# Optimization experiments

Hardware: AMD Instinct MI355X
Metric: run time of the kernel (lower is better)

Reference implementation:

```python
import jax, jax.numpy as jnp
import numpy as np
from jax.scipy.linalg import expm

B, S, D, E, K, NROT = 2, 2048, 1024, 8, 2, 3
EPS = 1e-5


def setup_inputs() -> dict:
    key = jax.random.key(0)
    ks = jax.random.split(key, 16)
    sc = 0.02
    x = jax.random.normal(ks[0], (B, S, D), jnp.float32)
    ln_gamma = 1.0 + sc * jax.random.normal(ks[1], (D,), jnp.float32)
    ln_beta = sc * jax.random.normal(ks[2], (D,), jnp.float32)
    abel_w = sc * jax.random.normal(ks[3], (D, D), jnp.float32)
    abel_b = sc * jax.random.normal(ks[4], (D,), jnp.float32)
    moe_gate_w = sc * jax.random.normal(ks[5], (D, E), jnp.float32)
    moe_gate_b = sc * jax.random.normal(ks[6], (E,), jnp.float32)
    ew1 = sc * jax.random.normal(ks[7], (E, D, 2 * D), jnp.float32)
    eb1 = sc * jax.random.normal(ks[8], (E, 2 * D), jnp.float32)
    ew2 = sc * jax.random.normal(ks[9], (E, 2 * D, D), jnp.float32)
    eb2 = sc * jax.random.normal(ks[10], (E, D), jnp.float32)
    g = sc * jax.random.normal(ks[11], (NROT, D, D), jnp.float32)
    gens = 0.5 * (g - jnp.swapaxes(g, -1, -2))  # skew-symmetric, as in reset_parameters
    gc_w = sc * jax.random.normal(ks[12], (2 * D, 1), jnp.float32)
    gc_b = sc * jax.random.normal(ks[13], (1,), jnp.float32)
    return dict(x=x, ln_gamma=ln_gamma, ln_beta=ln_beta, abel_w=abel_w, abel_b=abel_b,
                moe_gate_w=moe_gate_w, moe_gate_b=moe_gate_b, ew1=ew1, eb1=eb1,
                ew2=ew2, eb2=eb2, gens=gens, gc_w=gc_w, gc_b=gc_b)


def _gelu(x):
    return jax.nn.gelu(x, approximate=False)  # torch nn.GELU default = exact erf


def _forward(x, ln_gamma, ln_beta, abel_w, abel_b, moe_gate_w, moe_gate_b,
             ew1, eb1, ew2, eb2, gens, gc_w, gc_b):
    residual = x
    # LayerNorm
    mu = jnp.mean(x, axis=-1, keepdims=True)
    var = jnp.mean((x - mu) ** 2, axis=-1, keepdims=True)
    xn = (x - mu) * jax.lax.rsqrt(var + EPS) * ln_gamma + ln_beta
    # abel branch: Linear + GELU
    abel_out = _gelu(xn @ abel_w + abel_b)
    # MoE: dense all-experts compute, masked by top-k softmax weights
    logits = xn @ moe_gate_w + moe_gate_b                      # [B,S,E]
    topw, topi = jax.lax.top_k(logits, K)                      # [B,S,K]
    topw = jax.nn.softmax(topw, axis=-1)
    w_dense = jnp.sum(jax.nn.one_hot(topi, E, dtype=xn.dtype) * topw[..., None], axis=-2)  # [B,S,E]
    h = _gelu(jnp.einsum('bsd,edh->ebsh', xn, ew1) + eb1[:, None, None, :])  # [E,B,S,2D]
    eo = jnp.einsum('ebsh,ehd->ebsd', h, ew2) + eb2[:, None, None, :]        # [E,B,S,D]
    moe_out = jnp.einsum('ebsd,bse->bsd', eo, w_dense)
    # GeometricRotation: sequential matrix_exp rotations
    for i in range(NROT):
        moe_out = moe_out @ expm(gens[i])
    # gated residual mix
    combined = jnp.concatenate([abel_out, moe_out], axis=-1)
    gate = jax.nn.sigmoid(combined @ gc_w + gc_b)              # [B,S,1]
    mixed = abel_out * (1.0 - gate) + moe_out * gate
    return residual + mixed


def reference(x, ln_gamma, ln_beta, abel_w, abel_b, moe_gate_w, moe_gate_b,
              ew1, eb1, ew2, eb2, gens, gc_w, gc_b):
    return _forward(x, ln_gamma, ln_beta, abel_w, abel_b, moe_gate_w, moe_gate_b,
                    ew1, eb1, ew2, eb2, gens, gc_w, gc_b)
```

## Files before the change

kernel.cpp:

```cpp
#include <hip/hip_runtime.h>
#include <hip/hip_bf16.h>
#include <cstdint>
#include <cstddef>

#define DD   1024
#define DD2  2048
#define EE   8
#define NTOK 4096
#define CAPR 10240
#define MAXT1 72
#define MAXT2 56

typedef __bf16 bf16_t;
typedef __bf16 bf16x8 __attribute__((ext_vector_type(8)));
typedef __bf16 bf16x4 __attribute__((ext_vector_type(4)));
typedef float  f32x4v __attribute__((ext_vector_type(4)));

__device__ __forceinline__ float gelu_f(float v){
  const float t = v*(0.7978845608028654f + 0.0356774081f*v*v);
  const float u = __expf(2.0f*t);
  return __fdividef(v*u, 1.0f + u);
}

__device__ __forceinline__ void gload_lds16(const void* g, void* l){
  __builtin_amdgcn_global_load_lds(
    (const __attribute__((address_space(1))) unsigned int*)(uintptr_t)g,
    (__attribute__((address_space(3))) unsigned int*)(uintptr_t)l,
    16, 0, 0);
}

enum { EPI_GELU_F32=0, EPI_GELU_BF16=1, EPI_BIAS_BF16=2, EPI_SCALE_BF16=3,
       EPI_ADDV_BF16=4, EPI_BF16=5, EPI_F32=6 };

template<int BM,int BN,int WAVES,int EPI,bool TAB>
__global__ __launch_bounds__(WAVES*64)
void gemm_bt(const bf16_t* __restrict__ A, const bf16_t* __restrict__ Bt,
             const int N, const int K, const int gx, const int gy, const int gz,
             const long sAz, const long sBz, const long sOz,
             const int* __restrict__ tileE, const int* __restrict__ tileR,
             const int* __restrict__ ntp, const int* __restrict__ offp,
             const int* __restrict__ tokOf,
             const float* __restrict__ bias, const long sBias,
             const float alpha,
             const bf16_t* __restrict__ addv,
             const bf16_t* __restrict__ abelB, const float* __restrict__ abelBias,
             bf16_t* __restrict__ abelOut, const int aN, const int aGx,
             float* __restrict__ outF, bf16_t* __restrict__ outB)
{
  constexpr int BK = 32;
  constexpr int WROWS = WAVES/2;
  constexpr int WM = BM/WROWS, WN = BN/2;
  constexpr int FM = WM/16, FN = WN/16;
  constexpr int IA = BM/(16*WAVES), IB = BN/(16*WAVES);
  constexpr int NLD = IA + IB;
  __shared__ alignas(16) bf16_t sA[3][BM*BK];
  __shared__ alignas(16) bf16_t sB[3][BN*BK];

  int bx, by, bz; long ro = 0;
  if constexpr (TAB) {
    const int nwg = gx * gy;
    const int q = nwg >> 3, r = nwg & 7;
    const int k = blockIdx.x & 7, i = blockIdx.x >> 3;
    if (i >= q + (k < r ? 1 : 0)) return;
    const int l = k * q + (k < r ? k : r) + i;
    const int ti = l / gx; bx = l - ti*gx;
    if (ti >= ntp[0]) return;
    bz = tileE[ti]; by = 0;
    if (bz == EE) { if (bx >= aGx) return; ro = tileR[ti]; }
    else          { ro = (long)offp[bz] + tileR[ti]; }
  } else {
    const int nwg = gx * gy * gz;
    const int q = nwg >> 3, r = nwg & 7;
    const int k = blockIdx.x & 7, i = blockIdx.x >> 3;
    if (i >= q + (k < r ? 1 : 0)) return;
    const int l = k * q + (k < r ? k : r) + i;
    bx = l % gx; const int t2 = l / gx; by = t2 % gy; bz = t2 / gy;
  }

  const int z = bz;
  const bool abelT = TAB && (z == EE);
  int NN = abelT ? aN : N;
  const bool useTok = TAB && !abelT && (tokOf != nullptr);
  const bf16_t* Bp;
  const float*  bp;
  float*  oF = outF;
  bf16_t* oB;
  if (abelT) {
    Bp = abelB; bp = abelBias;
    oB = abelOut + ro * (long)aN;
  } else if constexpr (TAB) {
    Bp = Bt + (size_t)z * sBz;
    bp = bias ? bias + (size_t)z * sBias : nullptr;
    oB = outB + ro * (long)N;
  } else {
    Bp = Bt + (size_t)z * sBz;
    bp = bias ? bias + (size_t)z * sBias : nullptr;
    A += (size_t)z * sAz;
    oB = outB; if (oB) oB += (size_t)z * sOz;
    if (oF) oF += (size_t)z * sOz;
  }
  const bf16_t* vp = addv ? addv + (size_t)z * sOz : nullptr;

  const int tid = threadIdx.x;
  const int wid = tid >> 6, lid = tid & 63;
  const int wr = wid >> 1, wc = wid & 1;
  const int brow = (TAB ? 0 : by * BM), bcol = bx * BN;
  const int fr = lid & 15, fq = lid >> 4;
  const int rl = lid >> 2, qs = lid & 3;

  const char* aSrc[IA];
  const char* bSrc[IB];
  #pragma unroll
  for (int i = 0; i < IA; i++) {
    const int rloc = (wid*IA + i)*16 + rl;
    const int q = qs ^ ((rloc >> 1) & 3);
    const bf16_t* arow;
    if constexpr (TAB) {
      arow = useTok ? (A + (size_t)tokOf[ro + rloc] * K)
                    : (A + (size_t)(ro + rloc) * K);
    } else {
      arow = A + (size_t)(brow + rloc) * K;
    }
    aSrc[i] = (const char*)arow + q*16;
  }
  #pragma unroll
  for (int i = 0; i < IB; i++) {
    const int rloc = (wid*IB + i)*16 + rl;
    const int q = qs ^ ((rloc >> 1) & 3);
    bSrc[i] = (const char*)(Bp + (size_t)(bcol + rloc) * K) + q*16;
  }

  f32x4v acc[FM][FN] = {};

  auto stage = [&](int buf, int kt) {
    #pragma unroll
    for (int i = 0; i < IA; i++)
      gload_lds16(aSrc[i] + (size_t)kt*2, (char*)sA[buf] + (wid*IA + i)*1024);
    #pragma unroll
    for (int i = 0; i < IB; i++)
      gload_lds16(bSrc[i] + (size_t)kt*2, (char*)sB[buf] + (wid*IB + i)*1024);
  };

  stage(0, 0);
  stage(1, BK);
  const int nk = K / BK;
  int b0 = 0, b1 = 1, b2 = 2;

  for (int t = 0; t < nk; ++t) {
    if (t < nk - 1) asm volatile("s_waitcnt vmcnt(%0)" :: "i"(NLD) : "memory");
    else            asm volatile("s_waitcnt vmcnt(0)" ::: "memory");
    __builtin_amdgcn_s_barrier();
    __builtin_amdgcn_sched_barrier(0);
    if (t + 2 < nk) stage(b2, (t + 2)*BK);

    bf16x8 af[FM], bb[FN];
    #pragma unroll
    for (int mi = 0; mi < FM; mi++) {
      const int r2 = wr*WM + mi*16 + fr;
      const int q = fq ^ ((r2 >> 1) & 3);
      af[mi] = *(const bf16x8*)((const char*)sA[b0] + r2*64 + q*16);
    }
    #pragma unroll
    for (int ni = 0; ni < FN; ni++) {
      const int r2 = wc*WN + ni*16 + fr;
      const int q = fq ^ ((r2 >> 1) & 3);
      bb[ni] = *(const bf16x8*)((const char*)sB[b0] + r2*64 + q*16);
    }
    #pragma unroll
    for (int mi = 0; mi < FM; mi++)
      #pragma unroll
      for (int ni = 0; ni < FN; ni++)
        acc[mi][ni] = __builtin_amdgcn_mfma_f32_16x16x32_bf16(
            af[mi], bb[ni], acc[mi][ni], 0, 0, 0);

    const int tb_ = b0; b0 = b1; b1 = b2; b2 = tb_;
  }

  #pragma unroll
  for (int mi = 0; mi < FM; mi++) {
    #pragma unroll
    for (int ni = 0; ni < FN; ni++) {
      const int rg0 = brow + wr*WM + mi*16 + fq*4;
      const int cg  = bcol + wc*WN + ni*16 + fr;
      #pragma unroll
      for (int i = 0; i < 4; i++) {
        const int rg = rg0 + i;
        float v = acc[mi][ni][i];
        if constexpr (EPI == EPI_GELU_F32) {
          v += bp[cg];
          oF[(size_t)rg*NN + cg] = gelu_f(v);
        } else if constexpr (EPI == EPI_GELU_BF16) {
          v += bp[cg];
          oB[(size_t)rg*NN + cg] = (bf16_t)gelu_f(v);
        } else if constexpr (EPI == EPI_BIAS_BF16) {
          v += bp[cg];
          oB[(size_t)rg*NN + cg] = (bf16_t)v;
        } else if constexpr (EPI == EPI_SCALE_BF16) {
          oB[(size_t)rg*NN + cg] = (bf16_t)(v * alpha);
        } else if constexpr (EPI == EPI_ADDV_BF16) {
          oB[(size_t)rg*NN + cg] = (bf16_t)(v + (float)vp[(size_t)rg*NN + cg]);
        } else if constexpr (EPI == EPI_BF16) {
          oB[(size_t)rg*NN + cg] = (bf16_t)v;
        } else {
          oF[(size_t)rg*NN + cg] = v;
        }
      }
    }
  }
}

struct TRef { const float* src; bf16_t* dst; int R, C, bx, by; };

__device__ __forceinline__ TRef resolve256(
    int ti, const float* abel_w, bf16_t* abel_wT,
    const float* ew1, bf16_t* ew1T, const float* ew2, bf16_t* ew2T){
  TRef tr;
  if (ti < 64) {
    tr.src = abel_w; tr.dst = abel_wT; tr.R = DD; tr.C = DD;
    tr.bx = ti & 15; tr.by = ti >> 4;
  } else if (ti < 1088) {
    const int i = ti - 64, z = i >> 7, r = i & 127;
    tr.src = ew1 + (size_t)z*DD*DD2; tr.dst = ew1T + (size_t)z*DD2*DD;
    tr.R = DD; tr.C = DD2; tr.bx = r & 31; tr.by = r >> 5;
  } else {
    const int i = ti - 1088, z = i >> 7, r = i & 127;
    tr.src = ew2 + (size_t)z*DD2*DD; tr.dst = ew2T + (size_t)z*DD*DD2;
    tr.R = DD2; tr.C = DD; tr.bx = r & 15; tr.by = r >> 4;
  }
  return tr;
}

__global__ __launch_bounds__(256)
void pre_kernel(const float* __restrict__ x, const float* __restrict__ gamma,
                const float* __restrict__ beta, const float* __restrict__ gw,
                const float* __restrict__ gb,
                bf16_t* __restrict__ xnb, int2* __restrict__ ids,
                float2* __restrict__ wts,
                const float* __restrict__ abel_w, bf16_t* __restrict__ abel_wT,
                const float* __restrict__ ew1, bf16_t* __restrict__ ew1T,
                const float* __restrict__ ew2, bf16_t* __restrict__ ew2T,
                const float* __restrict__ gens, bf16_t* __restrict__ Hn)
{
  __shared__ bf16_t tb[64][260];
  __shared__ float redS[4], redQ[4], mv[2], pr[32];
  const int bid = blockIdx.x, tid = threadIdx.x;

  if (bid < 4096) {
    const int t = bid, j0 = tid*4;
    const int wid = tid >> 6, lid = tid & 63;
    const float4 v = *(const float4*)(x + (size_t)t*DD + j0);
    float s  = v.x + v.y + v.z + v.w;
    float ss = v.x*v.x + v.y*v.y + v.z*v.z + v.w*v.w;
    #pragma unroll
    for (int off = 32; off; off >>= 1) { s += __shfl_down(s, off); ss += __shfl_down(ss, off); }
    if (lid == 0) { redS[wid] = s; redQ[wid] = ss; }
    __syncthreads();
    if (tid == 0) {
      const float S1 = redS[0]+redS[1]+redS[2]+redS[3];
      const float S2 = redQ[0]+redQ[1]+redQ[2]+redQ[3];
      const float mu  = S1 * (1.0f/DD);
      const float var = S2 * (1.0f/DD) - mu*mu;
      mv[0] = mu; mv[1] = rsqrtf(var + 1e-5f);
    }
    __syncthreads();
    const float mu = mv[0], rstd = mv[1];
    const float4 g = *(const float4*)(gamma + j0);
    const float4 b = *(const float4*)(beta  + j0);
    float xn[4];
    xn[0] = (v.x-mu)*rstd*g.x + b.x;
    xn[1] = (v.y-mu)*rstd*g.y + b.y;
    xn[2] = (v.z-mu)*rstd*g.z + b.z;
    xn[3] = (v.w-mu)*rstd*g.w + b.w;
    bf16x4 ov; ov[0]=(bf16_t)xn[0]; ov[1]=(bf16_t)xn[1]; ov[2]=(bf16_t)xn[2]; ov[3]=(bf16_t)xn[3];
    *(bf16x4*)(xnb + (size_t)t*DD + j0) = ov;

    float p[8] = {0,0,0,0,0,0,0,0};
    #pragma unroll
    for (int i = 0; i < 4; i++) {
      const float4 a0 = *(const float4*)(gw + (size_t)(j0+i)*EE);
      const float4 a1 = *(const float4*)(gw + (size_t)(j0+i)*EE + 4);
      const float xv = xn[i];
      p[0]+=xv*a0.x; p[1]+=xv*a0.y; p[2]+=xv*a0.z; p[3]+=xv*a0.w;
      p[4]+=xv*a1.x; p[5]+=xv*a1.y; p[6]+=xv*a1.z; p[7]+=xv*a1.w;
    }
    #pragma unroll
    for (int off = 32; off; off >>= 1) {
      #pragma unroll
      for (int e = 0; e < 8; e++) p[e] += __shfl_down(p[e], off);
    }
    if (lid == 0) {
      #pragma unroll
      for (int e = 0; e < 8; e++) pr[wid*8 + e] = p[e];
    }
    __syncthreads();
    if (tid == 0) {
      float l[8];
      #pragma unroll
      for (int e = 0; e < 8; e++) l[e] = pr[e] + pr[8+e] + pr[16+e] + pr[24+e] + gb[e];
      int i1 = 0; float m1 = l[0];
      #pragma unroll
      for (int e = 1; e < 8; e++) if (l[e] > m1) { m1 = l[e]; i1 = e; }
      int i2 = 0; float m2 = -1e30f;
      #pragma unroll
      for (int e = 0; e < 8; e++) if (e != i1 && l[e] > m2) { m2 = l[e]; i2 = e; }
      const float wa = 1.0f/(1.0f + expf(m2 - m1));
      ids[t] = make_int2(i1, i2);
      wts[t] = make_float2(wa, 1.0f - wa);
    }
  } else if (bid < 6208) {
    const TRef tr = resolve256(bid - 4096, abel_w, abel_wT, ew1, ew1T, ew2, ew2T);
    const int lx = tid & 15, ly = tid >> 4;
    const int r0 = tr.by*256, c0 = tr.bx*64;
    #pragma unroll
    for (int i = 0; i < 16; i++) {
      const int r = ly + i*16;
      const float4 v = *(const float4*)(tr.src + (size_t)(r0 + r)*tr.C + c0 + lx*4);
      tb[lx*4+0][r] = (bf16_t)v.x;
      tb[lx*4+1][r] = (bf16_t)v.y;
      tb[lx*4+2][r] = (bf16_t)v.z;
      tb[lx*4+3][r] = (bf16_t)v.w;
    }
    __syncthreads();
    const int w = tid >> 6, l = tid & 63;
    #pragma unroll
    for (int i = 0; i < 16; i++) {
      const int c = w*16 + i;
      const bf16x4 o = *(const bf16x4*)(&tb[c][l*4]);
      *(bf16x4*)(tr.dst + (size_t)(c0 + c)*tr.R + r0 + l*4) = o;
    }
  } else {
    #pragma unroll
    for (int it = 0; it < 4; it++) {
      const long i4 = (((long)(bid - 6208)*4 + it)*256 + tid)*4;
      const float4 v = *(const float4*)(gens + i4);
      bf16x4 b; b[0]=(bf16_t)(-v.x); b[1]=(bf16_t)(-v.y);
      b[2]=(bf16_t)(-v.z); b[3]=(bf16_t)(-v.w);
      *(bf16x4*)(Hn + i4) = b;
    }
  }
}

__global__ __launch_bounds__(256)
void tb16_kernel(const bf16_t* __restrict__ Ut, bf16_t* __restrict__ Tb){
  __shared__ bf16_t tile[32][33];
  const bf16_t* src = Ut + (size_t)(1 - blockIdx.z) * DD * DD;
  bf16_t*       dst = Tb + (size_t)blockIdx.z * DD * DD;
  const int c0 = blockIdx.x*32, r0 = blockIdx.y*32;
  #pragma unroll
  for (int i = 0; i < 4; i++)
    tile[threadIdx.y + i*8][threadIdx.x] = src[(size_t)(r0 + threadIdx.y + i*8)*DD + c0 + threadIdx.x];
  __syncthreads();
  #pragma unroll
  for (int i = 0; i < 4; i++)
    dst[(size_t)(c0 + threadIdx.y + i*8)*DD + r0 + threadIdx.x] = tile[threadIdx.x][threadIdx.y + i*8];
}

__global__ __launch_bounds__(256)
void vw_kernel(const bf16_t* __restrict__ Hn, const bf16_t* __restrict__ H2,
               bf16_t* __restrict__ Vb, bf16_t* __restrict__ Wtb){
  const long i0 = ((long)blockIdx.x*256 + threadIdx.x)*4;
  const long rc = i0 % (long)(DD*DD);
  const int r = (int)(rc / DD), c0 = (int)(rc % DD);
  const bf16x4 h  = *(const bf16x4*)(Hn + i0);
  const bf16x4 h2 = *(const bf16x4*)(H2 + i0);
  bf16x4 v, w;
  #pragma unroll
  for (int j = 0; j < 4; j++) {
    const float d  = (r == c0 + j) ? 1.0f : 0.0f;
    const float fh = (float)h[j], f2 = (float)h2[j];
    v[j] = (bf16_t)(d + fh + f2*0.5f);
    w[j] = (bf16_t)(d*(1.0f/6.0f) - fh*(1.0f/24.0f) + f2*(1.0f/120.0f));
  }
  *(bf16x4*)(Vb  + i0) = v;
  *(bf16x4*)(Wtb + i0) = w;
}

__global__ __launch_bounds__(256)
void route_kernel(const int2* __restrict__ ids, int* __restrict__ slotA,
                  int* __restrict__ slotB, int* __restrict__ cnt,
                  int* __restrict__ off, int* __restrict__ tE1,
                  int* __restrict__ tR1, int* __restrict__ tE2,
                  int* __restrict__ tR2, int* __restrict__ ntp)
{
  const int tid = threadIdx.x;
  const int wid = tid >> 6, lid = tid & 63;
  __shared__ int wsum[EE][4];
  __shared__ int base[EE];
  if (tid < EE) base[tid] = 0;
  __syncthreads();
  const unsigned long long lt = (1ull << lid) - 1ull;
  for (int c0 = 0; c0 < NTOK; c0 += 256) {
    const int t = c0 + tid;
    const int2 id = ids[t];
    int pA = 0, pB = 0;
    #pragma unroll
    for (int e = 0; e < EE; e++) {
      const bool fA = (id.x == e), fB = (id.y == e);
      const unsigned long long mA = __ballot(fA);
      const unsigned long long mB = __ballot(fB);
      const int cA = __popcll(mA);
      if (lid == 0) wsum[e][wid] = cA + __popcll(mB);
      if (fA) pA = __popcll(mA & lt);
      if (fB) pB = cA + __popcll(mB & lt);
    }
    __syncthreads();
    int wbA = base[id.x], wbB = base[id.y];
    for (int w = 0; w < wid; w++) { wbA += wsum[id.x][w]; wbB += wsum[id.y][w]; }
    slotA[t] = wbA + pA;
    slotB[t] = wbB + pB;
    __syncthreads();
    if (tid < EE) base[tid] += wsum[tid][0]+wsum[tid][1]+wsum[tid][2]+wsum[tid][3];
    __syncthreads();
  }
  if (tid == 0) {
    int a = 0, n1 = 0, n2 = 0;
    for (int e = 0; e < EE; e++) {
      cnt[e] = base[e]; off[e] = a;
      for (int r2 = 0; r2 < base[e]; r2 += 128) { tE1[n1] = e; tR1[n1] = r2; n1++; }
      for (int r2 = 0; r2 < base[e]; r2 += 256) { tE2[n2] = e; tR2[n2] = r2; n2++; }
      a += (base[e] + 255) & ~255;
    }
    for (int m = 0; m < NTOK/256; m++) { tE2[n2] = EE; tR2[n2] = m*256; n2++; }
    ntp[0] = n1; ntp[1] = n2;
  }
}

__global__ __launch_bounds__(256)
void fill_tok_kernel(const int2* __restrict__ ids, const int* __restrict__ slotA,
                     const int* __restrict__ slotB, const int* __restrict__ off,
                     const int* __restrict__ cnt, int* __restrict__ tokOf){
  const int t = blockIdx.x*256 + threadIdx.x;
  const int2 id = ids[t];
  tokOf[off[id.x] + slotA[t]] = t;
  tokOf[off[id.y] + slotB[t]] = t;
  if (blockIdx.x == 0) {
    for (int e = 0; e < EE; e++) {
      const int c = cnt[e], o = off[e], al = (c + 255) & ~255;
      for (int p = c + threadIdx.x; p < al; p += 256) tokOf[o + p] = 0;
    }
  }
}

__global__ __launch_bounds__(256)
void combine_kernel(const bf16_t* __restrict__ Yg, const int2* __restrict__ ids,
                    const int* __restrict__ slotA, const int* __restrict__ slotB,
                    const int* __restrict__ off, const float2* __restrict__ wts,
                    bf16_t* __restrict__ Xa){
  const int t = blockIdx.x, j = threadIdx.x*4;
  const int2 id = ids[t];
  const float2 w = wts[t];
  const bf16x4 a = *(const bf16x4*)(Yg + (size_t)(off[id.x] + slotA[t])*DD + j);
  const bf16x4 b = *(const bf16x4*)(Yg + (size_t)(off[id.y] + slotB[t])*DD + j);
  bf16x4 o;
  #pragma unroll
  for (int i = 0; i < 4; i++) o[i] = (bf16_t)(w.x*(float)a[i] + w.y*(float)b[i]);
  *(bf16x4*)(Xa + (size_t)t*DD + j) = o;
}

__global__ __launch_bounds__(256)
void mix_kernel(const float* __restrict__ x, const bf16_t* __restrict__ abel,
                const float* __restrict__ rot, const float* __restrict__ gcw,
                const float* __restrict__ gcb, float* __restrict__ out)
{
  const int t = blockIdx.x, tid = threadIdx.x, j0 = tid*4;
  const int wid = tid >> 6, lid = tid & 63;
  const bf16x4 ab = *(const bf16x4*)(abel + (size_t)t*DD + j0);
  const float4 r  = *(const float4*)(rot  + (size_t)t*DD + j0);
  const float4 ga = *(const float4*)(gcw + j0);
  const float4 gr = *(const float4*)(gcw + DD + j0);
  const float a0 = (float)ab[0], a1 = (float)ab[1], a2 = (float)ab[2], a3 = (float)ab[3];
  float p = a0*ga.x + a1*ga.y + a2*ga.z + a3*ga.w
          + r.x*gr.x + r.y*gr.y + r.z*gr.z + r.w*gr.w;
  #pragma unroll
  for (int off = 32; off; off >>= 1) p += __shfl_down(p, off);
  __shared__ float red[4];
  __shared__ float gsh;
  if (lid == 0) red[wid] = p;
  __syncthreads();
  if (tid == 0) {
    const float P = red[0] + red[1] + red[2] + red[3] + gcb[0];
    gsh = 1.0f/(1.0f + expf(-P));
  }
  __syncthreads();
  const float gate = gsh, g1 = 1.0f - gate;
  const float4 xv = *(const float4*)(x + (size_t)t*DD + j0);
  float4 o;
  o.x = xv.x + a0*g1 + r.x*gate;
  o.y = xv.y + a1*g1 + r.y*gate;
  o.z = xv.z + a2*g1 + r.z*gate;
  o.w = xv.w + a3*g1 + r.w*gate;
  *(float4*)(out + (size_t)t*DD + j0) = o;
}

extern "C" void kernel_launch(void* const* d_in, const int* in_sizes, int n_in,
                              void* d_out, int out_size, void* d_ws, size_t ws_size,
                              hipStream_t stream)
{
  (void)in_sizes; (void)n_in; (void)out_size; (void)ws_size;
  const float* x      = (const float*)d_in[0];
  const float* ln_g   = (const float*)d_in[1];
  const float* ln_b   = (const float*)d_in[2];
  const float* abel_w = (const float*)d_in[3];
  const float* abel_b = (const float*)d_in[4];
  const float* gate_w = (const float*)d_in[5];
  const float* gate_b = (const float*)d_in[6];
  const float* ew1    = (const float*)d_in[7];
  const float* eb1    = (const float*)d_in[8];
  const float* ew2    = (const float*)d_in[9];
  const float* eb2    = (const float*)d_in[10];
  const float* gens   = (const float*)d_in[11];
  const float* gc_w   = (const float*)d_in[12];
  const float* gc_b   = (const float*)d_in[13];
  float* out = (float*)d_out;

  char* wsp = (char*)d_ws;
  auto alloc = [&](size_t bytes) -> char* {
    char* p = wsp; wsp += (bytes + 255) & ~(size_t)255; return p;
  };
  const size_t MB = 1u<<20;
  bf16_t* xnb   = (bf16_t*)alloc((size_t)NTOK*DD*2);
  int2*   ids   = (int2*)  alloc((size_t)NTOK*8);
  float2* wts   = (float2*)alloc((size_t)NTOK*8);
  int*    slotA = (int*)   alloc((size_t)NTOK*4);
  int*    slotB = (int*)   alloc((size_t)NTOK*4);
  int*    cnt   = (int*)   alloc(64);
  int*    off   = (int*)   alloc(64);
  int*    tE1   = (int*)   alloc(MAXT1*4);
  int*    tR1   = (int*)   alloc(MAXT1*4);
  int*    tE2   = (int*)   alloc(MAXT2*4);
  int*    tR2   = (int*)   alloc(MAXT2*4);
  int*    ntp   = (int*)   alloc(64);
  int*    tokOf = (int*)   alloc((size_t)CAPR*4);
  bf16_t* abel_wT = (bf16_t*)alloc((size_t)DD*DD*2);
  char*   UN      = alloc(64*MB);
  bf16_t* ew1T  = (bf16_t*)UN;
  bf16_t* ew2T  = (bf16_t*)(UN + 32*MB);
  bf16_t* Hn    = (bf16_t*)alloc((size_t)3*DD*DD*2);
  bf16_t* abelo = (bf16_t*)alloc((size_t)NTOK*DD*2);
  bf16_t* Yg    = (bf16_t*)alloc((size_t)CAPR*DD*2);
  bf16_t* Hg    = (bf16_t*)alloc((size_t)CAPR*DD2*2);
  bf16_t* Xa    = (bf16_t*)alloc((size_t)NTOK*DD*2);
  float*  rot   = (float*)Hg;
  bf16_t* H2  = (bf16_t*)(UN + 0*MB);
  bf16_t* H3  = (bf16_t*)(UN + 6*MB);
  bf16_t* Vb  = (bf16_t*)(UN + 12*MB);
  bf16_t* Wtb = (bf16_t*)(UN + 18*MB);
  bf16_t* Ut  = (bf16_t*)(UN + 24*MB);
  bf16_t* Tb  = (bf16_t*)(UN + 30*MB);
  bf16_t* Pb  = (bf16_t*)(UN + 34*MB);
  bf16_t* Rt  = (bf16_t*)(UN + 36*MB);
  const long D2 = (long)DD*DD;

  auto gflat = [](int gx, int gy, int gz) {
    const int nwg = gx*gy*gz; return 8 * ((nwg + 7) / 8);
  };

  pre_kernel<<<dim3(6976,1,1), 256, 0, stream>>>(
      x, ln_g, ln_b, gate_w, gate_b, xnb, ids, wts,
      abel_w, abel_wT, ew1, ew1T, ew2, ew2T, gens, Hn);

  route_kernel<<<dim3(1,1,1), 256, 0, stream>>>(ids, slotA, slotB, cnt, off,
                                                tE1, tR1, tE2, tR2, ntp);
  fill_tok_kernel<<<dim3(NTOK/256,1,1), 256, 0, stream>>>(ids, slotA, slotB, off, cnt, tokOf);

  gemm_bt<256,128,8,EPI_GELU_BF16,true><<<dim3(gflat(DD2/128, MAXT2, 1),1,1), 512, 0, stream>>>(
      xnb, ew1T, DD2, DD, DD2/128, MAXT2, 1, 0, (long)DD2*DD, 0,
      tE2, tR2, ntp + 1, off, tokOf, eb1, DD2, 1.0f, nullptr,
      abel_wT, abel_b, abelo, DD, DD/128, nullptr, Hg);
  gemm_bt<128,128,4,EPI_BIAS_BF16,true><<<dim3(gflat(DD/128, MAXT1, 1),1,1), 256, 0, stream>>>(
      Hg, ew2T, DD, DD2, DD/128, MAXT1, 1, 0, (long)DD*DD2, 0,
      tE1, tR1, ntp, off, nullptr, eb2, DD, 1.0f, nullptr,
      nullptr, nullptr, nullptr, 0, 0, nullptr, Yg);
  combine_kernel<<<dim3(NTOK,1,1), 256, 0, stream>>>(Yg, ids, slotA, slotB, off, wts, Xa);

  gemm_bt<64,64,4,EPI_SCALE_BF16,false><<<dim3(gflat(16,16,3),1,1), 256, 0, stream>>>(
      Hn, Hn, DD, DD, 16, 16, 3, D2, D2, D2, nullptr, nullptr, nullptr, nullptr,
      nullptr, nullptr, 0, -1.0f, nullptr,
      nullptr, nullptr, nullptr, 0, 0, nullptr, H2);
  gemm_bt<64,64,4,EPI_SCALE_BF16,false><<<dim3(gflat(16,16,3),1,1), 256, 0, stream>>>(
      H2, Hn, DD, DD, 16, 16, 3, D2, D2, D2, nullptr, nullptr, nullptr, nullptr,
      nullptr, nullptr, 0, -1.0f, nullptr,
      nullptr, nullptr, nullptr, 0, 0, nullptr, H3);
  vw_kernel<<<dim3(3*DD*DD/1024,1,1), 256, 0, stream>>>(Hn, H2, Vb, Wtb);
  gemm_bt<64,64,4,EPI_ADDV_BF16,false><<<dim3(gflat(16,16,3),1,1), 256, 0, stream>>>(
      H3, Wtb, DD, DD, 16, 16, 3, D2, D2, D2, nullptr, nullptr, nullptr, nullptr,
      nullptr, nullptr, 0, 1.0f, Vb,
      nullptr, nullptr, nullptr, 0, 0, nullptr, Ut);
  tb16_kernel<<<dim3(32,32,2), dim3(32,8,1), 0, stream>>>(Ut, Tb);
  gemm_bt<64,64,4,EPI_BF16,false><<<dim3(gflat(16,16,1),1,1), 256, 0, stream>>>(
      Ut + 2*D2, Tb, DD, DD, 16, 16, 1, 0, 0, 0, nullptr, nullptr, nullptr, nullptr,
      nullptr, nullptr, 0, 1.0f, nullptr,
      nullptr, nullptr, nullptr, 0, 0, nullptr, Pb);
  gemm_bt<64,64,4,EPI_BF16,false><<<dim3(gflat(16,16,1),1,1), 256, 0, stream>>>(
      Pb, Tb + D2, DD, DD, 16, 16, 1, 0, 0, 0, nullptr, nullptr, nullptr, nullptr,
      nullptr, nullptr, 0, 1.0f, nullptr,
      nullptr, nullptr, nullptr, 0, 0, nullptr, Rt);
  gemm_bt<128,128,4,EPI_F32,false><<<dim3(gflat(8,32,1),1,1), 256, 0, stream>>>(
      Xa, Rt, DD, DD, 8, 32, 1, 0, 0, 0, nullptr, nullptr, nullptr, nullptr,
      nullptr, nullptr, 0, 1.0f, nullptr,
      nullptr, nullptr, nullptr, 0, 0, rot, nullptr);

  mix_kernel<<<dim3(NTOK,1,1), 256, 0, stream>>>(x, abelo, rot, gc_w, gc_b, out);
}
```

Before: 341.1 us.

## Split prologue into weight-transpose and LayerNorm/gate kernels; retile rotation GEMM

```diff
diff --git a/kernel.cpp b/kernel.cpp
--- a/kernel.cpp
+++ b/kernel.cpp
@@ -209,134 +209,52 @@
   }
 }
 
-struct TRef { const float* src; bf16_t* dst; int R, C, bx, by; };
-
-__device__ __forceinline__ TRef resolve256(
-    int ti, const float* abel_w, bf16_t* abel_wT,
-    const float* ew1, bf16_t* ew1T, const float* ew2, bf16_t* ew2T){
-  TRef tr;
-  if (ti < 64) {
-    tr.src = abel_w; tr.dst = abel_wT; tr.R = DD; tr.C = DD;
-    tr.bx = ti & 15; tr.by = ti >> 4;
-  } else if (ti < 1088) {
-    const int i = ti - 64, z = i >> 7, r = i & 127;
-    tr.src = ew1 + (size_t)z*DD*DD2; tr.dst = ew1T + (size_t)z*DD2*DD;
-    tr.R = DD; tr.C = DD2; tr.bx = r & 31; tr.by = r >> 5;
+__device__ __forceinline__ void tcvt_tile(const float* __restrict__ src,
+                                          bf16_t* __restrict__ dst,
+                                          int R, int C, int bx, int by,
+                                          float (*t)[65]){
+  const int c0 = bx*64, r0 = by*64;
+  const int lx = threadIdx.x & 15, ly = threadIdx.x >> 4;
+  #pragma unroll
+  for (int i = 0; i < 4; i++) {
+    const int row = r0 + ly + i*16;
+    const float4 v = *(const float4*)(src + (size_t)row*C + c0 + lx*4);
+    t[ly + i*16][lx*4+0] = v.x; t[ly + i*16][lx*4+1] = v.y;
+    t[ly + i*16][lx*4+2] = v.z; t[ly + i*16][lx*4+3] = v.w;
+  }
+  __syncthreads();
+  #pragma unroll
+  for (int i = 0; i < 4; i++) {
+    const int c = c0 + ly + i*16;
+    bf16x4 o;
+    #pragma unroll
+    for (int j = 0; j < 4; j++) o[j] = (bf16_t)t[lx*4+j][ly + i*16];
+    *(bf16x4*)(dst + (size_t)c*R + r0 + lx*4) = o;
+  }
+}
+
+__global__ __launch_bounds__(256)
+void prep_kernel(const float* __restrict__ abel_w, bf16_t* __restrict__ abel_wT,
+                 const float* __restrict__ ew1, bf16_t* __restrict__ ew1T,
+                 const float* __restrict__ ew2, bf16_t* __restrict__ ew2T,
+                 const float* __restrict__ gens, bf16_t* __restrict__ Hn)
+{
+  __shared__ float t[64][65];
+  const int bid = blockIdx.x;
+  if (bid < 256) {
+    tcvt_tile(abel_w, abel_wT, DD, DD, bid & 15, bid >> 4, t);
+  } else if (bid < 4352) {
+    const int i = bid - 256, z = i >> 9, r = i & 511;
+    tcvt_tile(ew1 + (size_t)z*DD*DD2, ew1T + (size_t)z*DD2*DD, DD, DD2, r & 31, r >> 5, t);
+  } else if (bid < 8448) {
+    const int i = bid - 4352, z = i >> 9, r = i & 511;
+    tcvt_tile(ew2 + (size_t)z*DD2*DD, ew2T + (size_t)z*DD*DD2, DD2, DD, r & 15, r >> 4, t);
   } else {
-    const int i = ti - 1088, z = i >> 7, r = i & 127;
-    tr.src = ew2 + (size_t)z*DD2*DD; tr.dst = ew2T + (size_t)z*DD*DD2;
-    tr.R = DD2; tr.C = DD; tr.bx = r & 15; tr.by = r >> 4;
-  }
-  return tr;
-}
-
-__global__ __launch_bounds__(256)
-void pre_kernel(const float* __restrict__ x, const float* __restrict__ gamma,
-                const float* __restrict__ beta, const float* __restrict__ gw,
-                const float* __restrict__ gb,
-                bf16_t* __restrict__ xnb, int2* __restrict__ ids,
-                float2* __restrict__ wts,
-                const float* __restrict__ abel_w, bf16_t* __restrict__ abel_wT,
-                const float* __restrict__ ew1, bf16_t* __restrict__ ew1T,
-                const float* __restrict__ ew2, bf16_t* __restrict__ ew2T,
-                const float* __restrict__ gens, bf16_t* __restrict__ Hn)
-{
-  __shared__ bf16_t tb[64][260];
-  __shared__ float redS[4], redQ[4], mv[2], pr[32];
-  const int bid = blockIdx.x, tid = threadIdx.x;
-
-  if (bid < 4096) {
-    const int t = bid, j0 = tid*4;
-    const int wid = tid >> 6, lid = tid & 63;
-    const float4 v = *(const float4*)(x + (size_t)t*DD + j0);
-    float s  = v.x + v.y + v.z + v.w;
-    float ss = v.x*v.x + v.y*v.y + v.z*v.z + v.w*v.w;
-    #pragma unroll
-    for (int off = 32; off; off >>= 1) { s += __shfl_down(s, off); ss += __shfl_down(ss, off); }
-    if (lid == 0) { redS[wid] = s; redQ[wid] = ss; }
-    __syncthreads();
-    if (tid == 0) {
-      const float S1 = redS[0]+redS[1]+redS[2]+redS[3];
-      const float S2 = redQ[0]+redQ[1]+redQ[2]+redQ[3];
-      const float mu  = S1 * (1.0f/DD);
-      const float var = S2 * (1.0f/DD) - mu*mu;
-      mv[0] = mu; mv[1] = rsqrtf(var + 1e-5f);
-    }
-    __syncthreads();
-    const float mu = mv[0], rstd = mv[1];
-    const float4 g = *(const float4*)(gamma + j0);
-    const float4 b = *(const float4*)(beta  + j0);
-    float xn[4];
-    xn[0] = (v.x-mu)*rstd*g.x + b.x;
-    xn[1] = (v.y-mu)*rstd*g.y + b.y;
-    xn[2] = (v.z-mu)*rstd*g.z + b.z;
-    xn[3] = (v.w-mu)*rstd*g.w + b.w;
-    bf16x4 ov; ov[0]=(bf16_t)xn[0]; ov[1]=(bf16_t)xn[1]; ov[2]=(bf16_t)xn[2]; ov[3]=(bf16_t)xn[3];
-    *(bf16x4*)(xnb + (size_t)t*DD + j0) = ov;
-
-    float p[8] = {0,0,0,0,0,0,0,0};
-    #pragma unroll
-    for (int i = 0; i < 4; i++) {
-      const float4 a0 = *(const float4*)(gw + (size_t)(j0+i)*EE);
-      const float4 a1 = *(const float4*)(gw + (size_t)(j0+i)*EE + 4);
-      const float xv = xn[i];
-      p[0]+=xv*a0.x; p[1]+=xv*a0.y; p[2]+=xv*a0.z; p[3]+=xv*a0.w;
-      p[4]+=xv*a1.x; p[5]+=xv*a1.y; p[6]+=xv*a1.z; p[7]+=xv*a1.w;
-    }
-    #pragma unroll
-    for (int off = 32; off; off >>= 1) {
-      #pragma unroll
-      for (int e = 0; e < 8; e++) p[e] += __shfl_down(p[e], off);
-    }
-    if (lid == 0) {
-      #pragma unroll
-      for (int e = 0; e < 8; e++) pr[wid*8 + e] = p[e];
-    }
-    __syncthreads();
-    if (tid == 0) {
-      float l[8];
-      #pragma unroll
-      for (int e = 0; e < 8; e++) l[e] = pr[e] + pr[8+e] + pr[16+e] + pr[24+e] + gb[e];
-      int i1 = 0; float m1 = l[0];
-      #pragma unroll
-      for (int e = 1; e < 8; e++) if (l[e] > m1) { m1 = l[e]; i1 = e; }
-      int i2 = 0; float m2 = -1e30f;
-      #pragma unroll
-      for (int e = 0; e < 8; e++) if (e != i1 && l[e] > m2) { m2 = l[e]; i2 = e; }
-      const float wa = 1.0f/(1.0f + expf(m2 - m1));
-      ids[t] = make_int2(i1, i2);
-      wts[t] = make_float2(wa, 1.0f - wa);
-    }
-  } else if (bid < 6208) {
-    const TRef tr = resolve256(bid - 4096, abel_w, abel_wT, ew1, ew1T, ew2, ew2T);
-    const int lx = tid & 15, ly = tid >> 4;
-    const int r0 = tr.by*256, c0 = tr.bx*64;
-    #pragma unroll
-    for (int i = 0; i < 16; i++) {
-      const int r = ly + i*16;
-      const float4 v = *(const float4*)(tr.src + (size_t)(r0 + r)*tr.C + c0 + lx*4);
-      tb[lx*4+0][r] = (bf16_t)v.x;
-      tb[lx*4+1][r] = (bf16_t)v.y;
-      tb[lx*4+2][r] = (bf16_t)v.z;
-      tb[lx*4+3][r] = (bf16_t)v.w;
-    }
-    __syncthreads();
-    const int w = tid >> 6, l = tid & 63;
-    #pragma unroll
-    for (int i = 0; i < 16; i++) {
-      const int c = w*16 + i;
-      const bf16x4 o = *(const bf16x4*)(&tb[c][l*4]);
-      *(bf16x4*)(tr.dst + (size_t)(c0 + c)*tr.R + r0 + l*4) = o;
-    }
-  } else {
-    #pragma unroll
-    for (int it = 0; it < 4; it++) {
-      const long i4 = (((long)(bid - 6208)*4 + it)*256 + tid)*4;
-      const float4 v = *(const float4*)(gens + i4);
-      bf16x4 b; b[0]=(bf16_t)(-v.x); b[1]=(bf16_t)(-v.y);
-      b[2]=(bf16_t)(-v.z); b[3]=(bf16_t)(-v.w);
-      *(bf16x4*)(Hn + i4) = b;
-    }
+    const long i4 = ((long)(bid - 8448)*256 + threadIdx.x)*4;
+    const float4 v = *(const float4*)(gens + i4);
+    bf16x4 b; b[0]=(bf16_t)(-v.x); b[1]=(bf16_t)(-v.y);
+    b[2]=(bf16_t)(-v.z); b[3]=(bf16_t)(-v.w);
+    *(bf16x4*)(Hn + i4) = b;
   }
 }
 
@@ -373,6 +291,78 @@
   }
   *(bf16x4*)(Vb  + i0) = v;
   *(bf16x4*)(Wtb + i0) = w;
+}
+
+__global__ __launch_bounds__(256)
+void ln_gate_kernel(const float* __restrict__ x, const float* __restrict__ gamma,
+                    const float* __restrict__ beta, const float* __restrict__ gw,
+                    const float* __restrict__ gb,
+                    bf16_t* __restrict__ xnb, int2* __restrict__ ids,
+                    float2* __restrict__ wts)
+{
+  const int t = blockIdx.x, tid = threadIdx.x, j0 = tid*4;
+  const int wid = tid >> 6, lid = tid & 63;
+  const float4 v = *(const float4*)(x + (size_t)t*DD + j0);
+  float s  = v.x + v.y + v.z + v.w;
+  float ss = v.x*v.x + v.y*v.y + v.z*v.z + v.w*v.w;
+  #pragma unroll
+  for (int off = 32; off; off >>= 1) { s += __shfl_down(s, off); ss += __shfl_down(ss, off); }
+  __shared__ float redS[4], redQ[4], mv[2];
+  if (lid == 0) { redS[wid] = s; redQ[wid] = ss; }
+  __syncthreads();
+  if (tid == 0) {
+    const float S1 = redS[0]+redS[1]+redS[2]+redS[3];
+    const float S2 = redQ[0]+redQ[1]+redQ[2]+redQ[3];
+    const float mu  = S1 * (1.0f/DD);
+    const float var = S2 * (1.0f/DD) - mu*mu;
+    mv[0] = mu; mv[1] = rsqrtf(var + 1e-5f);
+  }
+  __syncthreads();
+  const float mu = mv[0], rstd = mv[1];
+  const float4 g = *(const float4*)(gamma + j0);
+  const float4 b = *(const float4*)(beta  + j0);
+  float xn[4];
+  xn[0] = (v.x-mu)*rstd*g.x + b.x;
+  xn[1] = (v.y-mu)*rstd*g.y + b.y;
+  xn[2] = (v.z-mu)*rstd*g.z + b.z;
+  xn[3] = (v.w-mu)*rstd*g.w + b.w;
+  bf16x4 ov; ov[0]=(bf16_t)xn[0]; ov[1]=(bf16_t)xn[1]; ov[2]=(bf16_t)xn[2]; ov[3]=(bf16_t)xn[3];
+  *(bf16x4*)(xnb + (size_t)t*DD + j0) = ov;
+
+  float p[8] = {0,0,0,0,0,0,0,0};
+  #pragma unroll
+  for (int i = 0; i < 4; i++) {
+    const float4 a0 = *(const float4*)(gw + (size_t)(j0+i)*EE);
+    const float4 a1 = *(const float4*)(gw + (size_t)(j0+i)*EE + 4);
+    const float xv = xn[i];
+    p[0]+=xv*a0.x; p[1]+=xv*a0.y; p[2]+=xv*a0.z; p[3]+=xv*a0.w;
+    p[4]+=xv*a1.x; p[5]+=xv*a1.y; p[6]+=xv*a1.z; p[7]+=xv*a1.w;
+  }
+  #pragma unroll
+  for (int off = 32; off; off >>= 1) {
+    #pragma unroll
+    for (int e = 0; e < 8; e++) p[e] += __shfl_down(p[e], off);
+  }
+  __shared__ float pr[32];
+  if (lid == 0) {
+    #pragma unroll
+    for (int e = 0; e < 8; e++) pr[wid*8 + e] = p[e];
+  }
+  __syncthreads();
+  if (tid == 0) {
+    float l[8];
+    #pragma unroll
+    for (int e = 0; e < 8; e++) l[e] = pr[e] + pr[8+e] + pr[16+e] + pr[24+e] + gb[e];
+    int i1 = 0; float m1 = l[0];
+    #pragma unroll
+    for (int e = 1; e < 8; e++) if (l[e] > m1) { m1 = l[e]; i1 = e; }
+    int i2 = 0; float m2 = -1e30f;
+    #pragma unroll
+    for (int e = 0; e < 8; e++) if (e != i1 && l[e] > m2) { m2 = l[e]; i2 = e; }
+    const float wa = 1.0f/(1.0f + expf(m2 - m1));
+    ids[t] = make_int2(i1, i2);
+    wts[t] = make_float2(wa, 1.0f - wa);
+  }
 }
 
 __global__ __launch_bounds__(256)
@@ -555,10 +545,10 @@
     const int nwg = gx*gy*gz; return 8 * ((nwg + 7) / 8);
   };
 
-  pre_kernel<<<dim3(6976,1,1), 256, 0, stream>>>(
-      x, ln_g, ln_b, gate_w, gate_b, xnb, ids, wts,
-      abel_w, abel_wT, ew1, ew1T, ew2, ew2T, gens, Hn);
-
+  prep_kernel<<<dim3(11520,1,1), 256, 0, stream>>>(abel_w, abel_wT, ew1, ew1T,
+                                                   ew2, ew2T, gens, Hn);
+  ln_gate_kernel<<<dim3(NTOK,1,1), 256, 0, stream>>>(x, ln_g, ln_b, gate_w, gate_b,
+                                                     xnb, ids, wts);
   route_kernel<<<dim3(1,1,1), 256, 0, stream>>>(ids, slotA, slotB, cnt, off,
                                                 tE1, tR1, tE2, tR2, ntp);
   fill_tok_kernel<<<dim3(NTOK/256,1,1), 256, 0, stream>>>(ids, slotA, slotB, off, cnt, tokOf);
@@ -595,8 +585,8 @@
       Pb, Tb + D2, DD, DD, 16, 16, 1, 0, 0, 0, nullptr, nullptr, nullptr, nullptr,
       nullptr, nullptr, 0, 1.0f, nullptr,
       nullptr, nullptr, nullptr, 0, 0, nullptr, Rt);
-  gemm_bt<128,128,4,EPI_F32,false><<<dim3(gflat(8,32,1),1,1), 256, 0, stream>>>(
-      Xa, Rt, DD, DD, 8, 32, 1, 0, 0, 0, nullptr, nullptr, nullptr, nullptr,
+  gemm_bt<128,64,4,EPI_F32,false><<<dim3(gflat(16,32,1),1,1), 256, 0, stream>>>(
+      Xa, Rt, DD, DD, 16, 32, 1, 0, 0, 0, nullptr, nullptr, nullptr, nullptr,
       nullptr, nullptr, 0, 1.0f, nullptr,
       nullptr, nullptr, nullptr, 0, 0, rot, nullptr);
 
```

New measurement: 339.6 us. About the same (-0.4%).
